# Kernel optimization log

Measured on AMD Instinct MI355X. Metric: run time of the kernel, lower is better.

## Reference

```python
import jax, jax.numpy as jnp
import numpy as np

N, E = 50000, 1600000
DIN, DOUT, H, DG = 128, 128, 8, 64
DH = DOUT // H  # per-head dim
NEG_SLOPE = 0.2


def _leaky(x):
    return jnp.where(x >= 0, x, NEG_SLOPE * x)


def setup_inputs() -> dict:
    key = jax.random.key(0)
    ks = jax.random.split(key, 9)
    row = jax.random.randint(ks[0], (E,), 0, N, dtype=jnp.int32)
    col = jax.random.randint(ks[1], (E,), 0, N, dtype=jnp.int32)
    val = jax.random.uniform(ks[2], (E,), dtype=jnp.float32)  # normalized adj values
    feat = jax.random.normal(ks[3], (N, DIN), dtype=jnp.float32)
    W = jax.random.normal(ks[4], (2, H, DIN, DH), dtype=jnp.float32) * 0.05
    b = jnp.zeros((2, H, DH), dtype=jnp.float32)
    att = jax.random.normal(ks[5], (H, 2 * DH), dtype=jnp.float32) * 0.1
    offset = jnp.zeros((2, DOUT), dtype=jnp.float32)
    scale = jnp.ones((2, DOUT), dtype=jnp.float32)
    weight_gate = jax.random.normal(ks[6], (2 * DIN + DG, H), dtype=jnp.float32) * 0.05
    weight_pool_gate = jax.random.normal(ks[7], (DIN, DG), dtype=jnp.float32) * 0.05
    return {"row": row, "col": col, "val": val, "feat": feat, "W": W, "b": b,
            "att": att, "offset": offset, "scale": scale,
            "weight_gate": weight_gate, "weight_pool_gate": weight_pool_gate}


def reference(row, col, val, feat, W, b, att, offset, scale, weight_gate, weight_pool_gate):
    # ---- gate values (GaAN eq. 3) ----
    zj = feat @ weight_pool_gate                                   # [N, DG]
    zmax = jax.ops.segment_max(zj[col], row, num_segments=N)       # max-pool over neighbors
    zmax = jnp.where(jnp.isfinite(zmax), zmax, 0.0)                # isolated nodes -> 0
    nmean = jax.ops.segment_sum(val[:, None] * feat[col], row, num_segments=N)  # spmm(adj, feat)
    gate = jnp.concatenate([feat, zmax, nmean], axis=1) @ weight_gate            # [N, H]
    # ---- per-order, per-head linear + relu ----
    fp = jax.nn.relu(jnp.einsum('nd,ohdk->onhk', feat, W) + b[:, None])  # [2, N, H, DH]
    f0, f1 = fp[0], fp[1]                                          # self / neighbor feats
    # ---- attention-weighted sparse aggregation ----
    a_self = _leaky(jnp.einsum('nhk,hk->nh', f0, att[:, :DH]))     # [N, H]
    a_neigh = _leaky(jnp.einsum('nhk,hk->nh', f1, att[:, DH:]))    # [N, H]
    w_edge = (a_self[row] + a_neigh[col]) * val[:, None]           # [E, H]
    agg = jax.ops.segment_sum(w_edge[:, :, None] * f1[col], row, num_segments=N)  # [N, H, DH]
    agg = agg * gate[:, :, None]                                   # gated heads
    h0 = f0.reshape(N, DOUT)
    h1 = agg.reshape(N, DOUT)
    # ---- per-node norm (torch _batch_norm over feature dim) ----
    def norm(x, s, o):
        mu = jnp.mean(x, axis=1, keepdims=True)
        var = jnp.var(x, axis=1, keepdims=True) + 1e-9
        return (x - mu) * s * jax.lax.rsqrt(var) + o
    h0 = norm(h0, scale[0], offset[0])
    h1 = norm(h1, scale[1], offset[1])
    return h0 + h1  # aggr == 'mean'
```

## Files before the change

kernel.cpp:

```cpp
#include <hip/hip_runtime.h>
#include <hip/hip_bf16.h>
#include <math.h>

#define DIN   128
#define DOUTC 128
#define HH    8
#define DHH   16
#define DGG   64
#define NCOLS 336
#define NC2   352
#define PH    176
#define PT    11
#define BSHIFT 7
#define CAP   6144
#define EPB   4096

typedef __attribute__((ext_vector_type(8))) short short8v;
typedef __attribute__((ext_vector_type(4))) float float4v;

__global__ void cvt_feat(const float* __restrict__ feat, __hip_bfloat16* __restrict__ featb, int total8) {
    int i = blockIdx.x * 256 + threadIdx.x;
    if (i < total8) {
        const float4* p = reinterpret_cast<const float4*>(feat) + 2 * (size_t)i;
        float4 x = p[0], y = p[1];
        union { __hip_bfloat16 h[8]; short8v v; } pk;
        pk.h[0] = __float2bfloat16(x.x); pk.h[1] = __float2bfloat16(x.y);
        pk.h[2] = __float2bfloat16(x.z); pk.h[3] = __float2bfloat16(x.w);
        pk.h[4] = __float2bfloat16(y.x); pk.h[5] = __float2bfloat16(y.y);
        pk.h[6] = __float2bfloat16(y.z); pk.h[7] = __float2bfloat16(y.w);
        reinterpret_cast<short8v*>(featb)[i] = pk.v;
    }
}

__global__ void prep2(const float* __restrict__ W, const float* __restrict__ b,
                      const float* __restrict__ Wg, const float* __restrict__ Wpg,
                      __hip_bfloat16* __restrict__ Btb, float* __restrict__ biasv) {
    int idx = blockIdx.x * 256 + threadIdx.x;
    if (idx < NC2 * DIN) {
        int col = idx >> 7;
        int k   = idx & 127;
        float v = 0.f;
        if (col < 256) {
            int o = col >> 7, jj = col & 127, h = jj >> 4, kd = jj & 15;
            v = W[((o * HH + h) * DIN + k) * DHH + kd];
        } else if (col < 320) {
            v = Wpg[k * DGG + (col - 256)];
        } else if (col < 328) {
            v = Wg[k * HH + (col - 320)];
        } else if (col < 336) {
            v = Wg[(192 + k) * HH + (col - 328)];
        }
        int u = (k >> 3) ^ (col & 7);
        Btb[col * DIN + u * 8 + (k & 7)] = __float2bfloat16(v);
    }
    if (idx < NC2) {
        float bv = 0.f;
        if (idx < 256) { int o = idx >> 7, jj = idx & 127; bv = b[(o * HH + (jj >> 4)) * DHH + (jj & 15)]; }
        biasv[idx] = bv;
    }
}

__global__ __launch_bounds__(256) void dense_mfma(
    const __hip_bfloat16* __restrict__ featb, const __hip_bfloat16* __restrict__ Btb,
    const float* __restrict__ biasv,
    float* __restrict__ f0, __hip_bfloat16* __restrict__ f1b, __hip_bfloat16* __restrict__ zjb,
    float* __restrict__ fg0, float* __restrict__ nodedat, int N) {
    __shared__ __align__(16) __hip_bfloat16 Bs[PH * DIN];
    int t   = threadIdx.x;
    int wid = t >> 6, l = t & 63;
    int r0  = blockIdx.x * 128 + wid * 32;
    int lr  = l & 15;
    int lk  = l >> 4;

    short8v a[2][4];
    #pragma unroll
    for (int rt = 0; rt < 2; ++rt) {
        int node = r0 + rt * 16 + lr;
        if (node >= N) node = N - 1;
        const short8v* ap = reinterpret_cast<const short8v*>(&featb[(size_t)node * DIN + lk * 8]);
        #pragma unroll
        for (int kk = 0; kk < 4; ++kk) a[rt][kk] = ap[kk * 4];
    }

    #pragma unroll
    for (int p = 0; p < 2; ++p) {
        __syncthreads();
        {
            const short8v* src = reinterpret_cast<const short8v*>(Btb + (size_t)p * PH * DIN);
            short8v* dst = reinterpret_cast<short8v*>(Bs);
            #pragma unroll
            for (int it = 0; it < 11; ++it) dst[it * 256 + t] = src[it * 256 + t];
        }
        __syncthreads();

        float4v acc[2][PT];
        #pragma unroll
        for (int rt = 0; rt < 2; ++rt)
            #pragma unroll
            for (int n = 0; n < PT; ++n) acc[rt][n] = (float4v)0.f;

        #pragma unroll
        for (int n = 0; n < PT; ++n) {
            int coll = n * 16 + lr;
            #pragma unroll
            for (int kk = 0; kk < 4; ++kk) {
                int u = (kk * 4 + lk) ^ (lr & 7);
                short8v bv = *reinterpret_cast<const short8v*>(&Bs[coll * DIN + u * 8]);
                acc[0][n] = __builtin_amdgcn_mfma_f32_16x16x32_bf16(a[0][kk], bv, acc[0][n], 0, 0, 0);
                acc[1][n] = __builtin_amdgcn_mfma_f32_16x16x32_bf16(a[1][kk], bv, acc[1][n], 0, 0, 0);
            }
        }

        #pragma unroll
        for (int rt = 0; rt < 2; ++rt) {
            #pragma unroll
            for (int rg = 0; rg < 4; ++rg) {
                int node = r0 + rt * 16 + lk * 4 + rg;
                if (node < N) {
                    #pragma unroll
                    for (int n = 0; n < PT; ++n) {
                        int col = p * PH + n * 16 + lr;
                        float v = acc[rt][n][rg] + biasv[col];
                        if (col < 128) {
                            v = v > 0.f ? v : 0.f;
                            f0[(size_t)node * DOUTC + col] = v;
                        } else if (col < 256) {
                            v = v > 0.f ? v : 0.f;
                            f1b[(size_t)node * DOUTC + (col - 128)] = __float2bfloat16(v);
                        } else if (col < 320) {
                            zjb[(size_t)node * DGG + (col - 256)] = __float2bfloat16(v);
                        } else if (col < 328) {
                            fg0[node * HH + (col - 320)] = v;
                        } else if (col < 336) {
                            nodedat[(size_t)node * 16 + 8 + (col - 328)] = v;
                        }
                    }
                }
            }
        }
    }
}

__global__ void attn_kernel(const float* __restrict__ f0, const __hip_bfloat16* __restrict__ f1b,
                            const float* __restrict__ att,
                            float* __restrict__ a_self, float* __restrict__ nodedat, int N) {
    int g = blockIdx.x * 256 + threadIdx.x;
    if (g >= N * 16) return;
    int node = g >> 4, u = g & 15, h = u >> 1;
    float s = 0.f;
    if ((u & 1) == 0) {
        const float4* p  = reinterpret_cast<const float4*>(&f0[(size_t)node * DOUTC + h * DHH]);
        const float*  av = &att[h * 32];
        #pragma unroll
        for (int q = 0; q < 4; ++q) {
            float4 x = p[q];
            s = fmaf(x.x, av[q * 4 + 0], fmaf(x.y, av[q * 4 + 1],
                fmaf(x.z, av[q * 4 + 2], fmaf(x.w, av[q * 4 + 3], s))));
        }
        s = (s >= 0.f) ? s : 0.2f * s;
        a_self[node * HH + h] = s;
    } else {
        const short8v* p = reinterpret_cast<const short8v*>(&f1b[(size_t)node * DOUTC + h * DHH]);
        const float*  av = &att[h * 32 + DHH];
        union { short8v v; __hip_bfloat16 hh[8]; } pk0, pk1;
        pk0.v = p[0]; pk1.v = p[1];
        #pragma unroll
        for (int q = 0; q < 8; ++q) s = fmaf(__bfloat162float(pk0.hh[q]), av[q], s);
        #pragma unroll
        for (int q = 0; q < 8; ++q) s = fmaf(__bfloat162float(pk1.hh[q]), av[8 + q], s);
        s = (s >= 0.f) ? s : 0.2f * s;
        nodedat[(size_t)node * 16 + h] = s;
    }
}

__global__ __launch_bounds__(256) void bhist(const int* __restrict__ row, int* __restrict__ gHist, int E) {
    __shared__ int hist[512];
    int tid = threadIdx.x;
    hist[tid] = 0; hist[tid + 256] = 0;
    __syncthreads();
    int e0 = blockIdx.x * EPB;
    #pragma unroll
    for (int k = 0; k < 16; ++k) {
        int e = e0 + k * 256 + tid;
        if (e < E) atomicAdd(&hist[row[e] >> BSHIFT], 1);
    }
    __syncthreads();
    if (hist[tid])       atomicAdd(&gHist[tid], hist[tid]);
    if (hist[tid + 256]) atomicAdd(&gHist[tid + 256], hist[tid + 256]);
}

__global__ __launch_bounds__(512) void bscan(const int* __restrict__ gHist, int* __restrict__ gBase,
                                             int* __restrict__ gCursor, int nbuck) {
    __shared__ int s[512];
    int tid = threadIdx.x;
    s[tid] = (tid < nbuck) ? gHist[tid] : 0;
    __syncthreads();
    for (int off = 1; off < 512; off <<= 1) {
        int add = (tid >= off) ? s[tid - off] : 0;
        __syncthreads();
        s[tid] += add;
        __syncthreads();
    }
    if (tid < nbuck) {
        int excl = (tid == 0) ? 0 : s[tid - 1];
        gBase[tid] = excl;
        gCursor[tid] = excl;
    }
}

__global__ __launch_bounds__(256) void bscatter(const int* __restrict__ row, const int* __restrict__ col,
                                                const float* __restrict__ val, int* __restrict__ gCursor,
                                                int2* __restrict__ ebuf, int E) {
    __shared__ int hist[512], base[512], rank[512];
    int tid = threadIdx.x;
    hist[tid] = 0; hist[tid + 256] = 0;
    __syncthreads();
    int e0 = blockIdx.x * EPB;
    #pragma unroll
    for (int k = 0; k < 16; ++k) {
        int e = e0 + k * 256 + tid;
        if (e < E) atomicAdd(&hist[row[e] >> BSHIFT], 1);
    }
    __syncthreads();
    if (hist[tid])       base[tid] = atomicAdd(&gCursor[tid], hist[tid]);
    if (hist[tid + 256]) base[tid + 256] = atomicAdd(&gCursor[tid + 256], hist[tid + 256]);
    rank[tid] = 0; rank[tid + 256] = 0;
    __syncthreads();
    #pragma unroll
    for (int k = 0; k < 16; ++k) {
        int e = e0 + k * 256 + tid;
        if (e < E) {
            int r = row[e];
            int bk = r >> BSHIFT;
            int loc = atomicAdd(&rank[bk], 1);
            int2 pk;
            pk.x = col[e] | ((r & 127) << 16);
            pk.y = __float_as_int(val[e]);
            ebuf[base[bk] + loc] = pk;
        }
    }
}

__global__ __launch_bounds__(256) void bsort(const int2* __restrict__ ebuf, const int* __restrict__ gHist,
                                             const int* __restrict__ gBase, int2* __restrict__ efin,
                                             int* __restrict__ rowptr, int N) {
    __shared__ int2 ent[CAP];
    __shared__ int h0[128], sc[128], rk[128];
    int b = blockIdx.x, tid = threadIdx.x;
    int cnt = gHist[b]; if (cnt > CAP) cnt = CAP;
    int base = gBase[b];
    if (tid < 128) h0[tid] = 0;
    __syncthreads();
    for (int i = tid; i < cnt; i += 256) {
        int2 e = ebuf[base + i];
        ent[i] = e;
        atomicAdd(&h0[(e.x >> 16) & 127], 1);
    }
    __syncthreads();
    if (tid < 128) sc[tid] = h0[tid];
    __syncthreads();
    for (int off = 1; off < 128; off <<= 1) {
        int add = (tid < 128 && tid >= off) ? sc[tid - off] : 0;
        __syncthreads();
        if (tid < 128) sc[tid] += add;
        __syncthreads();
    }
    if (tid < 128) {
        int excl = sc[tid] - h0[tid];
        rk[tid] = excl;
        int grow = b * 128 + tid;
        if (grow <= N) rowptr[grow] = base + excl;
    }
    __syncthreads();
    for (int i = tid; i < cnt; i += 256) {
        int2 e = ent[i];
        int dst = base + atomicAdd(&rk[(e.x >> 16) & 127], 1);
        efin[dst] = e;
    }
}

#define UN 8
__global__ __launch_bounds__(128) void edge_kernel(
    const int* __restrict__ rowptr, const int2* __restrict__ ef,
    const __hip_bfloat16* __restrict__ f1b, const __hip_bfloat16* __restrict__ zjb,
    const float* __restrict__ a_self, const float* __restrict__ nodedat,
    const float* __restrict__ fg0, const float* __restrict__ Wg,
    const float* __restrict__ f0, const float* __restrict__ scale, const float* __restrict__ offset,
    float* __restrict__ out) {
    int r = blockIdx.x;
    int t = threadIdx.x;
    int start = rowptr[r], end = rowptr[r + 1];

    __shared__ float lds_z[64];
    __shared__ float lds_n8[8];
    __shared__ float lds_gate[8];

    float accA0 = 0.f, accA1 = 0.f, accZ = -INFINITY, accN8 = 0.f;
    int h = t >> 3;
    float asr = 0.f;
    if (t < 64) asr = a_self[r * HH + h];
    int j = t - 64;

    for (int i = start; i < end; i += UN) {
        int   c[UN]; float v[UN]; bool ok[UN];
        #pragma unroll
        for (int u = 0; u < UN; ++u) {
            int idx = i + u;
            ok[u] = idx < end;
            int2 eu = ef[ok[u] ? idx : (end - 1)];
            c[u] = eu.x & 0xFFFF;
            v[u] = ok[u] ? __int_as_float(eu.y) : 0.f;
        }
        if (t < 64) {
            float an[UN];
            #pragma unroll
            for (int u = 0; u < UN; ++u) an[u] = nodedat[(size_t)c[u] * 16 + h];
            __hip_bfloat162 f2[UN];
            #pragma unroll
            for (int u = 0; u < UN; ++u)
                f2[u] = *reinterpret_cast<const __hip_bfloat162*>(&f1b[(size_t)c[u] * DOUTC + 2 * t]);
            #pragma unroll
            for (int u = 0; u < UN; ++u) {
                float w = (asr + an[u]) * v[u];
                accA0 = fmaf(w, __bfloat162float(f2[u].x), accA0);
                accA1 = fmaf(w, __bfloat162float(f2[u].y), accA1);
            }
        } else {
            float z[UN];
            #pragma unroll
            for (int u = 0; u < UN; ++u) z[u] = __bfloat162float(zjb[(size_t)c[u] * DGG + j]);
            #pragma unroll
            for (int u = 0; u < UN; ++u) if (ok[u]) accZ = fmaxf(accZ, z[u]);
            if (j < 8) {
                float g2[UN];
                #pragma unroll
                for (int u = 0; u < UN; ++u) g2[u] = nodedat[(size_t)c[u] * 16 + 8 + j];
                #pragma unroll
                for (int u = 0; u < UN; ++u) accN8 = fmaf(v[u], g2[u], accN8);
            }
        }
    }

    if (t >= 64) {
        lds_z[j] = (end > start) ? accZ : 0.f;
        if (j < 8) lds_n8[j] = accN8;
    }
    __syncthreads();

    if (t < 8) {
        float g = fg0[r * HH + t] + lds_n8[t];
        #pragma unroll
        for (int k = 0; k < 64; ++k) g = fmaf(lds_z[k], Wg[(128 + k) * HH + t], g);
        lds_gate[t] = g;
    }
    __syncthreads();

    if (t < 64) {
        float gh  = lds_gate[h];
        float h1x = accA0 * gh, h1y = accA1 * gh;
        float2 f0v = *reinterpret_cast<const float2*>(&f0[r * DOUTC + 2 * t]);
        float s0  = f0v.x + f0v.y;
        float s0q = f0v.x * f0v.x + f0v.y * f0v.y;
        float s1  = h1x + h1y;
        float s1q = h1x * h1x + h1y * h1y;
        #pragma unroll
        for (int off = 32; off > 0; off >>= 1) {
            s0  += __shfl_xor(s0,  off);
            s0q += __shfl_xor(s0q, off);
            s1  += __shfl_xor(s1,  off);
            s1q += __shfl_xor(s1q, off);
        }
        float mu0  = s0 * (1.f / 128.f), mu1 = s1 * (1.f / 128.f);
        float rs0  = rsqrtf(s0q * (1.f / 128.f) - mu0 * mu0 + 1e-9f);
        float rs1  = rsqrtf(s1q * (1.f / 128.f) - mu1 * mu1 + 1e-9f);
        float2 sc0 = *reinterpret_cast<const float2*>(&scale[2 * t]);
        float2 sc1 = *reinterpret_cast<const float2*>(&scale[128 + 2 * t]);
        float2 of0 = *reinterpret_cast<const float2*>(&offset[2 * t]);
        float2 of1 = *reinterpret_cast<const float2*>(&offset[128 + 2 * t]);
        float2 o2;
        o2.x = (f0v.x - mu0) * sc0.x * rs0 + of0.x + (h1x - mu1) * sc1.x * rs1 + of1.x;
        o2.y = (f0v.y - mu0) * sc0.y * rs0 + of0.y + (h1y - mu1) * sc1.y * rs1 + of1.y;
        *reinterpret_cast<float2*>(&out[r * DOUTC + 2 * t]) = o2;
    }
}

extern "C" void kernel_launch(void* const* d_in, const int* in_sizes, int n_in,
                              void* d_out, int out_size, void* d_ws, size_t ws_size,
                              hipStream_t stream) {
    const int*   row  = (const int*)  d_in[0];
    const int*   col  = (const int*)  d_in[1];
    const float* val  = (const float*)d_in[2];
    const float* feat = (const float*)d_in[3];
    const float* W    = (const float*)d_in[4];
    const float* b    = (const float*)d_in[5];
    const float* att  = (const float*)d_in[6];
    const float* offs = (const float*)d_in[7];
    const float* scal = (const float*)d_in[8];
    const float* Wg   = (const float*)d_in[9];
    const float* Wpg  = (const float*)d_in[10];
    float* out = (float*)d_out;

    const int E = in_sizes[0];
    const int N = in_sizes[3] / DIN;
    const int NBUCK = (N + 127) >> BSHIFT;
    const int NEBLK = (E + EPB - 1) / EPB;

    char* ws = (char*)d_ws;
    size_t off = 0;
    auto alloc = [&](size_t bytes) { size_t o = off; off = (off + bytes + 255) & ~(size_t)255; return o; };

    __hip_bfloat16* featb = (__hip_bfloat16*)(ws + alloc((size_t)N * DIN * 2));
    __hip_bfloat16* Btb   = (__hip_bfloat16*)(ws + alloc((size_t)NC2 * DIN * 2));
    float* biasv   = (float*)(ws + alloc(NC2 * 4));
    float* f0      = (float*)(ws + alloc((size_t)N * DOUTC * 4));
    __hip_bfloat16* f1b = (__hip_bfloat16*)(ws + alloc((size_t)N * DOUTC * 2));
    __hip_bfloat16* zjb = (__hip_bfloat16*)(ws + alloc((size_t)N * DGG * 2));
    float* a_self  = (float*)(ws + alloc((size_t)N * HH * 4));
    float* nodedat = (float*)(ws + alloc((size_t)N * 16 * 4));
    float* fg0     = (float*)(ws + alloc((size_t)N * HH * 4));
    int*   rowptr  = (int*)  (ws + alloc((size_t)(N + 1) * 4));
    int*   gHist   = (int*)  (ws + alloc(512 * 4));
    int*   gBase   = (int*)  (ws + alloc(512 * 4));
    int*   gCursor = (int*)  (ws + alloc(512 * 4));
    int2*  ebuf    = (int2*) (ws + alloc((size_t)E * 8));
    int2*  efin    = (int2*) (ws + alloc((size_t)E * 8));

    cvt_feat<<<(N * DIN / 8 + 255) / 256, 256, 0, stream>>>(feat, featb, N * DIN / 8);
    prep2<<<(NC2 * DIN + 255) / 256, 256, 0, stream>>>(W, b, Wg, Wpg, Btb, biasv);
    dense_mfma<<<(N + 127) / 128, 256, 0, stream>>>(featb, Btb, biasv, f0, f1b, zjb, fg0, nodedat, N);
    attn_kernel<<<(N * 16 + 255) / 256, 256, 0, stream>>>(f0, f1b, att, a_self, nodedat, N);
    hipMemsetAsync(gHist, 0, 512 * 4, stream);
    bhist<<<NEBLK, 256, 0, stream>>>(row, gHist, E);
    bscan<<<1, 512, 0, stream>>>(gHist, gBase, gCursor, NBUCK);
    bscatter<<<NEBLK, 256, 0, stream>>>(row, col, val, gCursor, ebuf, E);
    bsort<<<NBUCK, 256, 0, stream>>>(ebuf, gHist, gBase, efin, rowptr, N);
    edge_kernel<<<N, 128, 0, stream>>>(rowptr, efin, f1b, zjb, a_self, nodedat,
                                       fg0, Wg, f0, scal, offs, out);
}
```

Baseline: 321.1 us.

## Merge setup and histogram kernels, grid-stride edge kernel, smaller MFMA tiles

Merges feature conversion, weight packing and the row histogram into one launch; the histogram now writes per-block partials instead of using global atomics, which also removes the memset. The attention kernel and bucket scan share a second launch. The dense MFMA kernel handles 64 rows per block instead of 128, and the edge kernel loops over rows with a grid stride across N/8 blocks and splits each row's edges into a full unrolled main loop plus a scalar tail. This cuts launch count and per-block overhead but lowers reuse of the weight tile in dense_mfma, and the histogram now runs on only 64 blocks.

```diff
diff --git a/kernel.cpp b/kernel.cpp
--- a/kernel.cpp
+++ b/kernel.cpp
@@ -7,56 +7,68 @@
 #define HH    8
 #define DHH   16
 #define DGG   64
-#define NCOLS 336
 #define NC2   352
 #define PH    176
 #define PT    11
 #define BSHIFT 7
 #define CAP   6144
-#define EPB   4096
+#define HB    64
 
 typedef __attribute__((ext_vector_type(8))) short short8v;
 typedef __attribute__((ext_vector_type(4))) float float4v;
 
-__global__ void cvt_feat(const float* __restrict__ feat, __hip_bfloat16* __restrict__ featb, int total8) {
-    int i = blockIdx.x * 256 + threadIdx.x;
-    if (i < total8) {
-        const float4* p = reinterpret_cast<const float4*>(feat) + 2 * (size_t)i;
-        float4 x = p[0], y = p[1];
-        union { __hip_bfloat16 h[8]; short8v v; } pk;
-        pk.h[0] = __float2bfloat16(x.x); pk.h[1] = __float2bfloat16(x.y);
-        pk.h[2] = __float2bfloat16(x.z); pk.h[3] = __float2bfloat16(x.w);
-        pk.h[4] = __float2bfloat16(y.x); pk.h[5] = __float2bfloat16(y.y);
-        pk.h[6] = __float2bfloat16(y.z); pk.h[7] = __float2bfloat16(y.w);
-        reinterpret_cast<short8v*>(featb)[i] = pk.v;
-    }
-}
-
-__global__ void prep2(const float* __restrict__ W, const float* __restrict__ b,
-                      const float* __restrict__ Wg, const float* __restrict__ Wpg,
-                      __hip_bfloat16* __restrict__ Btb, float* __restrict__ biasv) {
-    int idx = blockIdx.x * 256 + threadIdx.x;
-    if (idx < NC2 * DIN) {
-        int col = idx >> 7;
-        int k   = idx & 127;
-        float v = 0.f;
-        if (col < 256) {
-            int o = col >> 7, jj = col & 127, h = jj >> 4, kd = jj & 15;
-            v = W[((o * HH + h) * DIN + k) * DHH + kd];
-        } else if (col < 320) {
-            v = Wpg[k * DGG + (col - 256)];
-        } else if (col < 328) {
-            v = Wg[k * HH + (col - 320)];
-        } else if (col < 336) {
-            v = Wg[(192 + k) * HH + (col - 328)];
-        }
-        int u = (k >> 3) ^ (col & 7);
-        Btb[col * DIN + u * 8 + (k & 7)] = __float2bfloat16(v);
-    }
-    if (idx < NC2) {
-        float bv = 0.f;
-        if (idx < 256) { int o = idx >> 7, jj = idx & 127; bv = b[(o * HH + (jj >> 4)) * DHH + (jj & 15)]; }
-        biasv[idx] = bv;
+__global__ __launch_bounds__(256) void setup_kernel(
+    const float* __restrict__ feat, const float* __restrict__ W, const float* __restrict__ b,
+    const float* __restrict__ Wg, const float* __restrict__ Wpg, const int* __restrict__ row,
+    __hip_bfloat16* __restrict__ featb, __hip_bfloat16* __restrict__ Btb, float* __restrict__ biasv,
+    int* __restrict__ gHistP, int total8, int cvtB, int prepB, int E, int EH) {
+    int bid = blockIdx.x, tid = threadIdx.x;
+    if (bid < cvtB) {
+        int i = bid * 256 + tid;
+        if (i < total8) {
+            const float4* p = reinterpret_cast<const float4*>(feat) + 2 * (size_t)i;
+            float4 x = p[0], y = p[1];
+            union { __hip_bfloat16 h[8]; short8v v; } pk;
+            pk.h[0] = __float2bfloat16(x.x); pk.h[1] = __float2bfloat16(x.y);
+            pk.h[2] = __float2bfloat16(x.z); pk.h[3] = __float2bfloat16(x.w);
+            pk.h[4] = __float2bfloat16(y.x); pk.h[5] = __float2bfloat16(y.y);
+            pk.h[6] = __float2bfloat16(y.z); pk.h[7] = __float2bfloat16(y.w);
+            reinterpret_cast<short8v*>(featb)[i] = pk.v;
+        }
+    } else if (bid < cvtB + prepB) {
+        int idx = (bid - cvtB) * 256 + tid;
+        if (idx < NC2 * DIN) {
+            int col = idx >> 7;
+            int k   = idx & 127;
+            float v = 0.f;
+            if (col < 256) {
+                int o = col >> 7, jj = col & 127, h = jj >> 4, kd = jj & 15;
+                v = W[((o * HH + h) * DIN + k) * DHH + kd];
+            } else if (col < 320) {
+                v = Wpg[k * DGG + (col - 256)];
+            } else if (col < 328) {
+                v = Wg[k * HH + (col - 320)];
+            } else if (col < 336) {
+                v = Wg[(192 + k) * HH + (col - 328)];
+            }
+            int u = (k >> 3) ^ (col & 7);
+            Btb[col * DIN + u * 8 + (k & 7)] = __float2bfloat16(v);
+        }
+        if (idx < NC2) {
+            float bv = 0.f;
+            if (idx < 256) { int o = idx >> 7, jj = idx & 127; bv = b[(o * HH + (jj >> 4)) * DHH + (jj & 15)]; }
+            biasv[idx] = bv;
+        }
+    } else {
+        __shared__ int hist[512];
+        int hb = bid - cvtB - prepB;
+        hist[tid] = 0; hist[tid + 256] = 0;
+        __syncthreads();
+        int e0 = hb * EH, e1 = e0 + EH; if (e1 > E) e1 = E;
+        for (int e = e0 + tid; e < e1; e += 256) atomicAdd(&hist[row[e] >> BSHIFT], 1);
+        __syncthreads();
+        gHistP[hb * 512 + tid] = hist[tid];
+        gHistP[hb * 512 + tid + 256] = hist[tid + 256];
     }
 }
 
@@ -68,18 +80,17 @@
     __shared__ __align__(16) __hip_bfloat16 Bs[PH * DIN];
     int t   = threadIdx.x;
     int wid = t >> 6, l = t & 63;
-    int r0  = blockIdx.x * 128 + wid * 32;
+    int r0  = blockIdx.x * 64 + wid * 16;
     int lr  = l & 15;
     int lk  = l >> 4;
 
-    short8v a[2][4];
-    #pragma unroll
-    for (int rt = 0; rt < 2; ++rt) {
-        int node = r0 + rt * 16 + lr;
+    short8v a[4];
+    {
+        int node = r0 + lr;
         if (node >= N) node = N - 1;
         const short8v* ap = reinterpret_cast<const short8v*>(&featb[(size_t)node * DIN + lk * 8]);
         #pragma unroll
-        for (int kk = 0; kk < 4; ++kk) a[rt][kk] = ap[kk * 4];
+        for (int kk = 0; kk < 4; ++kk) a[kk] = ap[kk * 4];
     }
 
     #pragma unroll
@@ -93,11 +104,9 @@
         }
         __syncthreads();
 
-        float4v acc[2][PT];
+        float4v acc[PT];
         #pragma unroll
-        for (int rt = 0; rt < 2; ++rt)
-            #pragma unroll
-            for (int n = 0; n < PT; ++n) acc[rt][n] = (float4v)0.f;
+        for (int n = 0; n < PT; ++n) acc[n] = (float4v)0.f;
 
         #pragma unroll
         for (int n = 0; n < PT; ++n) {
@@ -106,34 +115,30 @@
             for (int kk = 0; kk < 4; ++kk) {
                 int u = (kk * 4 + lk) ^ (lr & 7);
                 short8v bv = *reinterpret_cast<const short8v*>(&Bs[coll * DIN + u * 8]);
-                acc[0][n] = __builtin_amdgcn_mfma_f32_16x16x32_bf16(a[0][kk], bv, acc[0][n], 0, 0, 0);
-                acc[1][n] = __builtin_amdgcn_mfma_f32_16x16x32_bf16(a[1][kk], bv, acc[1][n], 0, 0, 0);
+                acc[n] = __builtin_amdgcn_mfma_f32_16x16x32_bf16(a[kk], bv, acc[n], 0, 0, 0);
             }
         }
 
         #pragma unroll
-        for (int rt = 0; rt < 2; ++rt) {
-            #pragma unroll
-            for (int rg = 0; rg < 4; ++rg) {
-                int node = r0 + rt * 16 + lk * 4 + rg;
-                if (node < N) {
-                    #pragma unroll
-                    for (int n = 0; n < PT; ++n) {
-                        int col = p * PH + n * 16 + lr;
-                        float v = acc[rt][n][rg] + biasv[col];
-                        if (col < 128) {
-                            v = v > 0.f ? v : 0.f;
-                            f0[(size_t)node * DOUTC + col] = v;
-                        } else if (col < 256) {
-                            v = v > 0.f ? v : 0.f;
-                            f1b[(size_t)node * DOUTC + (col - 128)] = __float2bfloat16(v);
-                        } else if (col < 320) {
-                            zjb[(size_t)node * DGG + (col - 256)] = __float2bfloat16(v);
-                        } else if (col < 328) {
-                            fg0[node * HH + (col - 320)] = v;
-                        } else if (col < 336) {
-                            nodedat[(size_t)node * 16 + 8 + (col - 328)] = v;
-                        }
+        for (int rg = 0; rg < 4; ++rg) {
+            int node = r0 + lk * 4 + rg;
+            if (node < N) {
+                #pragma unroll
+                for (int n = 0; n < PT; ++n) {
+                    int col = p * PH + n * 16 + lr;
+                    float v = acc[n][rg] + biasv[col];
+                    if (col < 128) {
+                        v = v > 0.f ? v : 0.f;
+                        f0[(size_t)node * DOUTC + col] = v;
+                    } else if (col < 256) {
+                        v = v > 0.f ? v : 0.f;
+                        f1b[(size_t)node * DOUTC + (col - 128)] = __float2bfloat16(v);
+                    } else if (col < 320) {
+                        zjb[(size_t)node * DGG + (col - 256)] = __float2bfloat16(v);
+                    } else if (col < 328) {
+                        fg0[node * HH + (col - 320)] = v;
+                    } else if (col < 336) {
+                        nodedat[(size_t)node * 16 + 8 + (col - 328)] = v;
                     }
                 }
             }
@@ -141,73 +146,60 @@
     }
 }
 
-__global__ void attn_kernel(const float* __restrict__ f0, const __hip_bfloat16* __restrict__ f1b,
-                            const float* __restrict__ att,
-                            float* __restrict__ a_self, float* __restrict__ nodedat, int N) {
-    int g = blockIdx.x * 256 + threadIdx.x;
-    if (g >= N * 16) return;
-    int node = g >> 4, u = g & 15, h = u >> 1;
-    float s = 0.f;
-    if ((u & 1) == 0) {
-        const float4* p  = reinterpret_cast<const float4*>(&f0[(size_t)node * DOUTC + h * DHH]);
-        const float*  av = &att[h * 32];
+__global__ __launch_bounds__(512) void mid_kernel(
+    const float* __restrict__ f0, const __hip_bfloat16* __restrict__ f1b,
+    const float* __restrict__ att, float* __restrict__ a_self, float* __restrict__ nodedat,
+    const int* __restrict__ gHistP, int* __restrict__ gHist, int* __restrict__ gBase,
+    int* __restrict__ gCursor, int N, int attnB) {
+    int bid = blockIdx.x, tid = threadIdx.x;
+    if (bid < attnB) {
+        int g = bid * 512 + tid;
+        if (g >= N * 16) return;
+        int node = g >> 4, u = g & 15, h = u >> 1;
+        float s = 0.f;
+        if ((u & 1) == 0) {
+            const float4* p  = reinterpret_cast<const float4*>(&f0[(size_t)node * DOUTC + h * DHH]);
+            const float*  av = &att[h * 32];
+            #pragma unroll
+            for (int q = 0; q < 4; ++q) {
+                float4 x = p[q];
+                s = fmaf(x.x, av[q * 4 + 0], fmaf(x.y, av[q * 4 + 1],
+                    fmaf(x.z, av[q * 4 + 2], fmaf(x.w, av[q * 4 + 3], s))));
+            }
+            s = (s >= 0.f) ? s : 0.2f * s;
+            a_self[node * HH + h] = s;
+        } else {
+            const short8v* p = reinterpret_cast<const short8v*>(&f1b[(size_t)node * DOUTC + h * DHH]);
+            const float*  av = &att[h * 32 + DHH];
+            union { short8v v; __hip_bfloat16 hh[8]; } pk0, pk1;
+            pk0.v = p[0]; pk1.v = p[1];
+            #pragma unroll
+            for (int q = 0; q < 8; ++q) s = fmaf(__bfloat162float(pk0.hh[q]), av[q], s);
+            #pragma unroll
+            for (int q = 0; q < 8; ++q) s = fmaf(__bfloat162float(pk1.hh[q]), av[8 + q], s);
+            s = (s >= 0.f) ? s : 0.2f * s;
+            nodedat[(size_t)node * 16 + h] = s;
+        }
+    } else {
+        __shared__ int s[512];
+        int v = 0;
         #pragma unroll
-        for (int q = 0; q < 4; ++q) {
-            float4 x = p[q];
-            s = fmaf(x.x, av[q * 4 + 0], fmaf(x.y, av[q * 4 + 1],
-                fmaf(x.z, av[q * 4 + 2], fmaf(x.w, av[q * 4 + 3], s))));
-        }
-        s = (s >= 0.f) ? s : 0.2f * s;
-        a_self[node * HH + h] = s;
-    } else {
-        const short8v* p = reinterpret_cast<const short8v*>(&f1b[(size_t)node * DOUTC + h * DHH]);
-        const float*  av = &att[h * 32 + DHH];
-        union { short8v v; __hip_bfloat16 hh[8]; } pk0, pk1;
-        pk0.v = p[0]; pk1.v = p[1];
-        #pragma unroll
-        for (int q = 0; q < 8; ++q) s = fmaf(__bfloat162float(pk0.hh[q]), av[q], s);
-        #pragma unroll
-        for (int q = 0; q < 8; ++q) s = fmaf(__bfloat162float(pk1.hh[q]), av[8 + q], s);
-        s = (s >= 0.f) ? s : 0.2f * s;
-        nodedat[(size_t)node * 16 + h] = s;
-    }
-}
-
-__global__ __launch_bounds__(256) void bhist(const int* __restrict__ row, int* __restrict__ gHist, int E) {
-    __shared__ int hist[512];
-    int tid = threadIdx.x;
-    hist[tid] = 0; hist[tid + 256] = 0;
-    __syncthreads();
-    int e0 = blockIdx.x * EPB;
-    #pragma unroll
-    for (int k = 0; k < 16; ++k) {
-        int e = e0 + k * 256 + tid;
-        if (e < E) atomicAdd(&hist[row[e] >> BSHIFT], 1);
-    }
-    __syncthreads();
-    if (hist[tid])       atomicAdd(&gHist[tid], hist[tid]);
-    if (hist[tid + 256]) atomicAdd(&gHist[tid + 256], hist[tid + 256]);
-}
-
-__global__ __launch_bounds__(512) void bscan(const int* __restrict__ gHist, int* __restrict__ gBase,
-                                             int* __restrict__ gCursor, int nbuck) {
-    __shared__ int s[512];
-    int tid = threadIdx.x;
-    s[tid] = (tid < nbuck) ? gHist[tid] : 0;
-    __syncthreads();
-    for (int off = 1; off < 512; off <<= 1) {
-        int add = (tid >= off) ? s[tid - off] : 0;
-        __syncthreads();
-        s[tid] += add;
-        __syncthreads();
-    }
-    if (tid < nbuck) {
-        int excl = (tid == 0) ? 0 : s[tid - 1];
+        for (int s8 = 0; s8 < HB; ++s8) v += gHistP[s8 * 512 + tid];
+        gHist[tid] = v;
+        s[tid] = v; __syncthreads();
+        for (int off = 1; off < 512; off <<= 1) {
+            int add = (tid >= off) ? s[tid - off] : 0;
+            __syncthreads();
+            s[tid] += add;
+            __syncthreads();
+        }
+        int excl = s[tid] - v;
         gBase[tid] = excl;
         gCursor[tid] = excl;
     }
 }
 
+#define EPB   4096
 __global__ __launch_bounds__(256) void bscatter(const int* __restrict__ row, const int* __restrict__ col,
                                                 const float* __restrict__ val, int* __restrict__ gCursor,
                                                 int2* __restrict__ ebuf, int E) {
@@ -286,101 +278,116 @@
     const float* __restrict__ a_self, const float* __restrict__ nodedat,
     const float* __restrict__ fg0, const float* __restrict__ Wg,
     const float* __restrict__ f0, const float* __restrict__ scale, const float* __restrict__ offset,
-    float* __restrict__ out) {
-    int r = blockIdx.x;
+    float* __restrict__ out, int N, int gstride) {
     int t = threadIdx.x;
-    int start = rowptr[r], end = rowptr[r + 1];
+    int h = t >> 3;
+    int j = t - 64;
 
     __shared__ float lds_z[64];
     __shared__ float lds_n8[8];
     __shared__ float lds_gate[8];
 
-    float accA0 = 0.f, accA1 = 0.f, accZ = -INFINITY, accN8 = 0.f;
-    int h = t >> 3;
-    float asr = 0.f;
-    if (t < 64) asr = a_self[r * HH + h];
-    int j = t - 64;
-
-    for (int i = start; i < end; i += UN) {
-        int   c[UN]; float v[UN]; bool ok[UN];
-        #pragma unroll
-        for (int u = 0; u < UN; ++u) {
-            int idx = i + u;
-            ok[u] = idx < end;
-            int2 eu = ef[ok[u] ? idx : (end - 1)];
-            c[u] = eu.x & 0xFFFF;
-            v[u] = ok[u] ? __int_as_float(eu.y) : 0.f;
-        }
+    for (int r = blockIdx.x; r < N; r += gstride) {
+        int start = rowptr[r], end = rowptr[r + 1];
+
+        float accA0 = 0.f, accA1 = 0.f, accZ = -INFINITY, accN8 = 0.f;
+        float asr = 0.f;
+        if (t < 64) asr = a_self[r * HH + h];
+
+        int i = start;
+        for (; i + UN <= end; i += UN) {
+            int   c[UN]; float v[UN];
+            #pragma unroll
+            for (int u = 0; u < UN; ++u) {
+                int2 eu = ef[i + u];
+                c[u] = eu.x & 0xFFFF;
+                v[u] = __int_as_float(eu.y);
+            }
+            if (t < 64) {
+                float an[UN];
+                #pragma unroll
+                for (int u = 0; u < UN; ++u) an[u] = nodedat[(size_t)c[u] * 16 + h];
+                __hip_bfloat162 f2[UN];
+                #pragma unroll
+                for (int u = 0; u < UN; ++u)
+                    f2[u] = *reinterpret_cast<const __hip_bfloat162*>(&f1b[(size_t)c[u] * DOUTC + 2 * t]);
+                #pragma unroll
+                for (int u = 0; u < UN; ++u) {
+                    float w = (asr + an[u]) * v[u];
+                    accA0 = fmaf(w, __bfloat162float(f2[u].x), accA0);
+                    accA1 = fmaf(w, __bfloat162float(f2[u].y), accA1);
+                }
+            } else {
+                float z[UN];
+                #pragma unroll
+                for (int u = 0; u < UN; ++u) z[u] = __bfloat162float(zjb[(size_t)c[u] * DGG + j]);
+                #pragma unroll
+                for (int u = 0; u < UN; ++u) accZ = fmaxf(accZ, z[u]);
+                if (j < 8) {
+                    float g2[UN];
+                    #pragma unroll
+                    for (int u = 0; u < UN; ++u) g2[u] = nodedat[(size_t)c[u] * 16 + 8 + j];
+                    #pragma unroll
+                    for (int u = 0; u < UN; ++u) accN8 = fmaf(v[u], g2[u], accN8);
+                }
+            }
+        }
+        for (; i < end; ++i) {
+            int2 eu = ef[i];
+            int   c = eu.x & 0xFFFF;
+            float v = __int_as_float(eu.y);
+            if (t < 64) {
+                float w = (asr + nodedat[(size_t)c * 16 + h]) * v;
+                __hip_bfloat162 f2 = *reinterpret_cast<const __hip_bfloat162*>(&f1b[(size_t)c * DOUTC + 2 * t]);
+                accA0 = fmaf(w, __bfloat162float(f2.x), accA0);
+                accA1 = fmaf(w, __bfloat162float(f2.y), accA1);
+            } else {
+                accZ = fmaxf(accZ, __bfloat162float(zjb[(size_t)c * DGG + j]));
+                if (j < 8) accN8 = fmaf(v, nodedat[(size_t)c * 16 + 8 + j], accN8);
+            }
+        }
+
+        if (t >= 64) {
+            lds_z[j] = (end > start) ? accZ : 0.f;
+            if (j < 8) lds_n8[j] = accN8;
+        }
+        __syncthreads();
+
+        if (t < 8) {
+            float g = fg0[r * HH + t] + lds_n8[t];
+            #pragma unroll
+            for (int k = 0; k < 64; ++k) g = fmaf(lds_z[k], Wg[(128 + k) * HH + t], g);
+            lds_gate[t] = g;
+        }
+        __syncthreads();
+
         if (t < 64) {
-            float an[UN];
-            #pragma unroll
-            for (int u = 0; u < UN; ++u) an[u] = nodedat[(size_t)c[u] * 16 + h];
-            __hip_bfloat162 f2[UN];
-            #pragma unroll
-            for (int u = 0; u < UN; ++u)
-                f2[u] = *reinterpret_cast<const __hip_bfloat162*>(&f1b[(size_t)c[u] * DOUTC + 2 * t]);
-            #pragma unroll
-            for (int u = 0; u < UN; ++u) {
-                float w = (asr + an[u]) * v[u];
-                accA0 = fmaf(w, __bfloat162float(f2[u].x), accA0);
-                accA1 = fmaf(w, __bfloat162float(f2[u].y), accA1);
-            }
-        } else {
-            float z[UN];
-            #pragma unroll
-            for (int u = 0; u < UN; ++u) z[u] = __bfloat162float(zjb[(size_t)c[u] * DGG + j]);
-            #pragma unroll
-            for (int u = 0; u < UN; ++u) if (ok[u]) accZ = fmaxf(accZ, z[u]);
-            if (j < 8) {
-                float g2[UN];
-                #pragma unroll
-                for (int u = 0; u < UN; ++u) g2[u] = nodedat[(size_t)c[u] * 16 + 8 + j];
-                #pragma unroll
-                for (int u = 0; u < UN; ++u) accN8 = fmaf(v[u], g2[u], accN8);
-            }
-        }
-    }
-
-    if (t >= 64) {
-        lds_z[j] = (end > start) ? accZ : 0.f;
-        if (j < 8) lds_n8[j] = accN8;
-    }
-    __syncthreads();
-
-    if (t < 8) {
-        float g = fg0[r * HH + t] + lds_n8[t];
-        #pragma unroll
-        for (int k = 0; k < 64; ++k) g = fmaf(lds_z[k], Wg[(128 + k) * HH + t], g);
-        lds_gate[t] = g;
-    }
-    __syncthreads();
-
-    if (t < 64) {
-        float gh  = lds_gate[h];
-        float h1x = accA0 * gh, h1y = accA1 * gh;
-        float2 f0v = *reinterpret_cast<const float2*>(&f0[r * DOUTC + 2 * t]);
-        float s0  = f0v.x + f0v.y;
-        float s0q = f0v.x * f0v.x + f0v.y * f0v.y;
-        float s1  = h1x + h1y;
-        float s1q = h1x * h1x + h1y * h1y;
-        #pragma unroll
-        for (int off = 32; off > 0; off >>= 1) {
-            s0  += __shfl_xor(s0,  off);
-            s0q += __shfl_xor(s0q, off);
-            s1  += __shfl_xor(s1,  off);
-            s1q += __shfl_xor(s1q, off);
-        }
-        float mu0  = s0 * (1.f / 128.f), mu1 = s1 * (1.f / 128.f);
-        float rs0  = rsqrtf(s0q * (1.f / 128.f) - mu0 * mu0 + 1e-9f);
-        float rs1  = rsqrtf(s1q * (1.f / 128.f) - mu1 * mu1 + 1e-9f);
-        float2 sc0 = *reinterpret_cast<const float2*>(&scale[2 * t]);
-        float2 sc1 = *reinterpret_cast<const float2*>(&scale[128 + 2 * t]);
-        float2 of0 = *reinterpret_cast<const float2*>(&offset[2 * t]);
-        float2 of1 = *reinterpret_cast<const float2*>(&offset[128 + 2 * t]);
-        float2 o2;
-        o2.x = (f0v.x - mu0) * sc0.x * rs0 + of0.x + (h1x - mu1) * sc1.x * rs1 + of1.x;
-        o2.y = (f0v.y - mu0) * sc0.y * rs0 + of0.y + (h1y - mu1) * sc1.y * rs1 + of1.y;
-        *reinterpret_cast<float2*>(&out[r * DOUTC + 2 * t]) = o2;
+            float gh  = lds_gate[h];
+            float h1x = accA0 * gh, h1y = accA1 * gh;
+            float2 f0v = *reinterpret_cast<const float2*>(&f0[r * DOUTC + 2 * t]);
+            float s0  = f0v.x + f0v.y;
+            float s0q = f0v.x * f0v.x + f0v.y * f0v.y;
+            float s1  = h1x + h1y;
+            float s1q = h1x * h1x + h1y * h1y;
+            #pragma unroll
+            for (int off = 32; off > 0; off >>= 1) {
+                s0  += __shfl_xor(s0,  off);
+                s0q += __shfl_xor(s0q, off);
+                s1  += __shfl_xor(s1,  off);
+                s1q += __shfl_xor(s1q, off);
+            }
+            float mu0  = s0 * (1.f / 128.f), mu1 = s1 * (1.f / 128.f);
+            float rs0  = rsqrtf(s0q * (1.f / 128.f) - mu0 * mu0 + 1e-9f);
+            float rs1  = rsqrtf(s1q * (1.f / 128.f) - mu1 * mu1 + 1e-9f);
+            float2 sc0 = *reinterpret_cast<const float2*>(&scale[2 * t]);
+            float2 sc1 = *reinterpret_cast<const float2*>(&scale[128 + 2 * t]);
+            float2 of0 = *reinterpret_cast<const float2*>(&offset[2 * t]);
+            float2 of1 = *reinterpret_cast<const float2*>(&offset[128 + 2 * t]);
+            float2 o2;
+            o2.x = (f0v.x - mu0) * sc0.x * rs0 + of0.x + (h1x - mu1) * sc1.x * rs1 + of1.x;
+            o2.y = (f0v.y - mu0) * sc0.y * rs0 + of0.y + (h1y - mu1) * sc1.y * rs1 + of1.y;
+            *reinterpret_cast<float2*>(&out[r * DOUTC + 2 * t]) = o2;
+        }
     }
 }
 
@@ -419,21 +426,26 @@
     float* nodedat = (float*)(ws + alloc((size_t)N * 16 * 4));
     float* fg0     = (float*)(ws + alloc((size_t)N * HH * 4));
     int*   rowptr  = (int*)  (ws + alloc((size_t)(N + 1) * 4));
+    int*   gHistP  = (int*)  (ws + alloc((size_t)HB * 512 * 4));
     int*   gHist   = (int*)  (ws + alloc(512 * 4));
     int*   gBase   = (int*)  (ws + alloc(512 * 4));
     int*   gCursor = (int*)  (ws + alloc(512 * 4));
     int2*  ebuf    = (int2*) (ws + alloc((size_t)E * 8));
     int2*  efin    = (int2*) (ws + alloc((size_t)E * 8));
 
-    cvt_feat<<<(N * DIN / 8 + 255) / 256, 256, 0, stream>>>(feat, featb, N * DIN / 8);
-    prep2<<<(NC2 * DIN + 255) / 256, 256, 0, stream>>>(W, b, Wg, Wpg, Btb, biasv);
-    dense_mfma<<<(N + 127) / 128, 256, 0, stream>>>(featb, Btb, biasv, f0, f1b, zjb, fg0, nodedat, N);
-    attn_kernel<<<(N * 16 + 255) / 256, 256, 0, stream>>>(f0, f1b, att, a_self, nodedat, N);
-    hipMemsetAsync(gHist, 0, 512 * 4, stream);
-    bhist<<<NEBLK, 256, 0, stream>>>(row, gHist, E);
-    bscan<<<1, 512, 0, stream>>>(gHist, gBase, gCursor, NBUCK);
+    const int total8 = N * DIN / 8;
+    const int cvtB = (total8 + 255) / 256;
+    const int prepB = (NC2 * DIN + 255) / 256;
+    const int EH = (E + HB - 1) / HB;
+    setup_kernel<<<cvtB + prepB + HB, 256, 0, stream>>>(
+        feat, W, b, Wg, Wpg, row, featb, Btb, biasv, gHistP, total8, cvtB, prepB, E, EH);
+    dense_mfma<<<(N + 63) / 64, 256, 0, stream>>>(featb, Btb, biasv, f0, f1b, zjb, fg0, nodedat, N);
+    const int attnB = (N * 16 + 511) / 512;
+    mid_kernel<<<attnB + 1, 512, 0, stream>>>(f0, f1b, att, a_self, nodedat,
+                                              gHistP, gHist, gBase, gCursor, N, attnB);
     bscatter<<<NEBLK, 256, 0, stream>>>(row, col, val, gCursor, ebuf, E);
     bsort<<<NBUCK, 256, 0, stream>>>(ebuf, gHist, gBase, efin, rowptr, N);
-    edge_kernel<<<N, 128, 0, stream>>>(rowptr, efin, f1b, zjb, a_self, nodedat,
-                                       fg0, Wg, f0, scal, offs, out);
-}
+    const int ge = (N + 7) / 8;
+    edge_kernel<<<ge, 128, 0, stream>>>(rowptr, efin, f1b, zjb, a_self, nodedat,
+                                        fg0, Wg, f0, scal, offs, out, N, ge);
+}
```

After: 817.2 us. +154.5%, slower.
